# Kernel tuning notes

Hardware: AMD Instinct MI355X
Metric: run time of the kernel (lower is better)

The kernel has to match this reference:

```python
import jax, jax.numpy as jnp
import numpy as np

EPS = 1e-16


def _grads4(x):
    """Four directional shift-differences with zero 'same' padding.

    Matches the fixed 3x3 depthwise conv kernels (cross-correlation):
      Gy: x[i-1,j]   - x[i+1,j]
      Gx: x[i,j-1]   - x[i,j+1]
      GD: x[i-1,j-1] - x[i+1,j+1]
      Gd: x[i-1,j+1] - x[i+1,j-1]
    x: [B, C, H, W]
    """
    B, C, H, W = x.shape
    xp = jnp.pad(x, ((0, 0), (0, 0), (1, 1), (1, 1)))  # zero pad like padding='same'
    gy = xp[:, :, 0:H,     1:W + 1] - xp[:, :, 2:H + 2, 1:W + 1]
    gx = xp[:, :, 1:H + 1, 0:W]     - xp[:, :, 1:H + 1, 2:W + 2]
    gD = xp[:, :, 0:H,     0:W]     - xp[:, :, 2:H + 2, 2:W + 2]
    gd = xp[:, :, 0:H,     2:W + 2] - xp[:, :, 2:H + 2, 0:W]
    return jnp.concatenate([gy, gx, gD, gd], axis=1)  # [B, 4C, H, W]


def setup_inputs() -> dict:
    key = jax.random.key(0)
    k1, k2 = jax.random.split(key)
    shape = (16, 6, 512, 512)
    outputs = jax.random.normal(k1, shape, dtype=jnp.float32)
    labels = jax.random.normal(k2, shape, dtype=jnp.float32)
    return {"outputs": outputs, "labels": labels}


def reference(outputs, labels):
    g_out = _grads4(outputs)
    g_lab = _grads4(labels)
    l1 = jnp.mean(jnp.abs(g_out - g_lab))
    return jnp.sqrt(l1 + EPS)
```

## Files before the change

### kernel.cpp

```cpp
#include <hip/hip_runtime.h>
#include <math.h>


#define NTHREADS 256
#define STRIP 8
#define WV 512
#define HT 512
#define PLANES 96
#define STRIPS_PER_PLANE (HT / STRIP)
#define TOTAL_WAVES (PLANES * STRIPS_PER_PLANE)
#define NBLOCKS (TOTAL_WAVES / (NTHREADS / 64))

struct Row {
    float d[8];
    float eL, eR;
};

__device__ __forceinline__ Row load_row(const float* __restrict__ ob,
                                         const float* __restrict__ lb,
                                         int r, int lane) {
    Row row;
    const size_t off = (size_t)r * WV;
    const float4 o0 = *reinterpret_cast<const float4*>(ob + off);
    const float4 o1 = *reinterpret_cast<const float4*>(ob + off + 4);
    const float4 l0 = *reinterpret_cast<const float4*>(lb + off);
    const float4 l1 = *reinterpret_cast<const float4*>(lb + off + 4);
    row.d[0] = o0.x - l0.x; row.d[1] = o0.y - l0.y;
    row.d[2] = o0.z - l0.z; row.d[3] = o0.w - l0.w;
    row.d[4] = o1.x - l1.x; row.d[5] = o1.y - l1.y;
    row.d[6] = o1.z - l1.z; row.d[7] = o1.w - l1.w;
    const float up = __shfl_up(row.d[7], 1, 64);
    const float dn = __shfl_down(row.d[0], 1, 64);
    row.eL = (lane == 0) ? 0.f : up;
    row.eR = (lane == 63) ? 0.f : dn;
    return row;
}

__device__ __forceinline__ Row zero_row() {
    Row row;
    #pragma unroll
    for (int k = 0; k < 8; ++k) row.d[k] = 0.f;
    row.eL = 0.f; row.eR = 0.f;
    return row;
}

__global__ __launch_bounds__(NTHREADS) void struct_loss_partial(
        const float* __restrict__ out_p, const float* __restrict__ lab_p,
        float* __restrict__ partial) {
    const int gwave = (blockIdx.x * NTHREADS + threadIdx.x) >> 6;
    const int lane  = threadIdx.x & 63;
    const int plane = gwave >> 6;
    const int row0  = (gwave & 63) * STRIP;

    const size_t base = (size_t)plane * (HT * WV) + lane * 8;
    const float* ob = out_p + base;
    const float* lb = lab_p + base;

    float acc = 0.f;

    Row rp = (row0 > 0) ? load_row(ob, lb, row0 - 1, lane) : zero_row();
    Row rc = load_row(ob, lb, row0, lane);

    #pragma unroll
    for (int rr = 0; rr < STRIP; ++rr) {
        const int r = row0 + rr;
        Row rn = (r + 1 < HT) ? load_row(ob, lb, r + 1, lane) : zero_row();

        #pragma unroll
        for (int k = 0; k < 8; ++k) {
            const float cL = (k > 0) ? rc.d[k - 1] : rc.eL;
            const float cR = (k < 7) ? rc.d[k + 1] : rc.eR;
            const float pL = (k > 0) ? rp.d[k - 1] : rp.eL;
            const float pR = (k < 7) ? rp.d[k + 1] : rp.eR;
            const float nL = (k > 0) ? rn.d[k - 1] : rn.eL;
            const float nR = (k < 7) ? rn.d[k + 1] : rn.eR;

            const float gy = rp.d[k] - rn.d[k];
            const float gx = cL - cR;
            const float gD = pL - nR;
            const float gd = pR - nL;
            acc += fabsf(gy) + fabsf(gx) + fabsf(gD) + fabsf(gd);
        }
        rp = rc;
        rc = rn;
    }

    #pragma unroll
    for (int off = 32; off > 0; off >>= 1)
        acc += __shfl_down(acc, off, 64);

    __shared__ float smem[NTHREADS / 64];
    const int wid = threadIdx.x >> 6;
    if (lane == 0) smem[wid] = acc;
    __syncthreads();
    if (threadIdx.x == 0) {
        float s = 0.f;
        #pragma unroll
        for (int w = 0; w < NTHREADS / 64; ++w) s += smem[w];
        partial[blockIdx.x] = s;
    }
}

__global__ __launch_bounds__(256) void struct_loss_final(
        const float* __restrict__ partial, float* __restrict__ out,
        int nparts, double inv_count) {
    double acc = 0.0;
    for (int i = threadIdx.x; i < nparts; i += blockDim.x)
        acc += (double)partial[i];
    #pragma unroll
    for (int off = 32; off > 0; off >>= 1)
        acc += __shfl_down(acc, off, 64);
    __shared__ double smem[4];
    const int lane = threadIdx.x & 63;
    const int wid  = threadIdx.x >> 6;
    if (lane == 0) smem[wid] = acc;
    __syncthreads();
    if (threadIdx.x == 0) {
        double s = smem[0] + smem[1] + smem[2] + smem[3];
        out[0] = (float)sqrt(s * inv_count + 1e-16);
    }
}

extern "C" void kernel_launch(void* const* d_in, const int* in_sizes, int n_in,
                              void* d_out, int out_size, void* d_ws, size_t ws_size,
                              hipStream_t stream) {
    const float* outputs = (const float*)d_in[0];
    const float* labels  = (const float*)d_in[1];
    float* out = (float*)d_out;
    float* partials = (float*)d_ws;

    const double inv_count = 1.0 / (16.0 * 24.0 * 512.0 * 512.0);

    struct_loss_partial<<<NBLOCKS, NTHREADS, 0, stream>>>(outputs, labels, partials);
    struct_loss_final<<<1, 256, 0, stream>>>(partials, out, NBLOCKS, inv_count);
}
```

Measured before the change: 45.46 us.

## Fuse final reduction via last-block atomic, prefetch rows ahead, halve strip height

Merges the separate final-reduction kernel into the main kernel with a threadfence plus atomic counter, so the last finishing block sums the partials; a memset resets the counter each call. Row loads are now issued one row ahead of their conversion to overlap memory latency with compute. Strip height drops from 8 to 4, doubling the wave count, which adds more occupancy but also more redundant halo-row loads. It also adds a memset launch and atomic serialization at the end.

```diff
diff --git a/kernel.cpp b/kernel.cpp
--- a/kernel.cpp
+++ b/kernel.cpp
@@ -3,32 +3,34 @@
 
 
 #define NTHREADS 256
-#define STRIP 8
+#define STRIP 4
 #define WV 512
 #define HT 512
 #define PLANES 96
-#define STRIPS_PER_PLANE (HT / STRIP)
-#define TOTAL_WAVES (PLANES * STRIPS_PER_PLANE)
+#define WAVES_PER_PLANE (HT / STRIP)
+#define TOTAL_WAVES (PLANES * WAVES_PER_PLANE)
 #define NBLOCKS (TOTAL_WAVES / (NTHREADS / 64))
 
-struct Row {
-    float d[8];
-    float eL, eR;
-};
+struct Raw { float4 o0, o1, l0, l1; };
+struct Row { float d[8]; float eL, eR; };
 
-__device__ __forceinline__ Row load_row(const float* __restrict__ ob,
-                                         const float* __restrict__ lb,
-                                         int r, int lane) {
+__device__ __forceinline__ Raw load_raw(const float* __restrict__ ob,
+                                        const float* __restrict__ lb, int r) {
+    Raw w;
+    const size_t off = (size_t)r * WV;
+    w.o0 = *reinterpret_cast<const float4*>(ob + off);
+    w.o1 = *reinterpret_cast<const float4*>(ob + off + 4);
+    w.l0 = *reinterpret_cast<const float4*>(lb + off);
+    w.l1 = *reinterpret_cast<const float4*>(lb + off + 4);
+    return w;
+}
+
+__device__ __forceinline__ Row convert(const Raw& w, int lane) {
     Row row;
-    const size_t off = (size_t)r * WV;
-    const float4 o0 = *reinterpret_cast<const float4*>(ob + off);
-    const float4 o1 = *reinterpret_cast<const float4*>(ob + off + 4);
-    const float4 l0 = *reinterpret_cast<const float4*>(lb + off);
-    const float4 l1 = *reinterpret_cast<const float4*>(lb + off + 4);
-    row.d[0] = o0.x - l0.x; row.d[1] = o0.y - l0.y;
-    row.d[2] = o0.z - l0.z; row.d[3] = o0.w - l0.w;
-    row.d[4] = o1.x - l1.x; row.d[5] = o1.y - l1.y;
-    row.d[6] = o1.z - l1.z; row.d[7] = o1.w - l1.w;
+    row.d[0] = w.o0.x - w.l0.x; row.d[1] = w.o0.y - w.l0.y;
+    row.d[2] = w.o0.z - w.l0.z; row.d[3] = w.o0.w - w.l0.w;
+    row.d[4] = w.o1.x - w.l1.x; row.d[5] = w.o1.y - w.l1.y;
+    row.d[6] = w.o1.z - w.l1.z; row.d[7] = w.o1.w - w.l1.w;
     const float up = __shfl_up(row.d[7], 1, 64);
     const float dn = __shfl_down(row.d[0], 1, 64);
     row.eL = (lane == 0) ? 0.f : up;
@@ -44,13 +46,14 @@
     return row;
 }
 
-__global__ __launch_bounds__(NTHREADS) void struct_loss_partial(
+__global__ __launch_bounds__(NTHREADS) void struct_loss(
         const float* __restrict__ out_p, const float* __restrict__ lab_p,
-        float* __restrict__ partial) {
+        float* __restrict__ partials, unsigned* __restrict__ counter,
+        float* __restrict__ out, double inv_count) {
     const int gwave = (blockIdx.x * NTHREADS + threadIdx.x) >> 6;
     const int lane  = threadIdx.x & 63;
-    const int plane = gwave >> 6;
-    const int row0  = (gwave & 63) * STRIP;
+    const int plane = gwave >> 7;
+    const int row0  = (gwave & (WAVES_PER_PLANE - 1)) * STRIP;
 
     const size_t base = (size_t)plane * (HT * WV) + lane * 8;
     const float* ob = out_p + base;
@@ -58,13 +61,25 @@
 
     float acc = 0.f;
 
-    Row rp = (row0 > 0) ? load_row(ob, lb, row0 - 1, lane) : zero_row();
-    Row rc = load_row(ob, lb, row0, lane);
+    Raw raw_p, raw_c, raw_n;
+    const bool has_p = (row0 > 0);
+    if (has_p) raw_p = load_raw(ob, lb, row0 - 1);
+    raw_c = load_raw(ob, lb, row0);
+    raw_n = load_raw(ob, lb, row0 + 1);
+
+    Row rp = has_p ? convert(raw_p, lane) : zero_row();
+    Row rc = convert(raw_c, lane);
 
     #pragma unroll
     for (int rr = 0; rr < STRIP; ++rr) {
         const int r = row0 + rr;
-        Row rn = (r + 1 < HT) ? load_row(ob, lb, r + 1, lane) : zero_row();
+
+        Raw raw_n2;
+        const bool has_n2 = (r + 2 < HT);
+        if (has_n2) raw_n2 = load_raw(ob, lb, r + 2);
+
+        Row rn;
+        if (r + 1 < HT) rn = convert(raw_n, lane); else rn = zero_row();
 
         #pragma unroll
         for (int k = 0; k < 8; ++k) {
@@ -83,6 +98,7 @@
         }
         rp = rc;
         rc = rn;
+        raw_n = raw_n2;
     }
 
     #pragma unroll
@@ -93,31 +109,36 @@
     const int wid = threadIdx.x >> 6;
     if (lane == 0) smem[wid] = acc;
     __syncthreads();
+
+    __shared__ bool amLast;
     if (threadIdx.x == 0) {
         float s = 0.f;
         #pragma unroll
         for (int w = 0; w < NTHREADS / 64; ++w) s += smem[w];
-        partial[blockIdx.x] = s;
+        partials[blockIdx.x] = s;
+        __threadfence();
+        const unsigned old = atomicAdd(counter, 1u);
+        amLast = (old == (unsigned)(NBLOCKS - 1));
     }
-}
+    __syncthreads();
 
-__global__ __launch_bounds__(256) void struct_loss_final(
-        const float* __restrict__ partial, float* __restrict__ out,
-        int nparts, double inv_count) {
-    double acc = 0.0;
-    for (int i = threadIdx.x; i < nparts; i += blockDim.x)
-        acc += (double)partial[i];
-    #pragma unroll
-    for (int off = 32; off > 0; off >>= 1)
-        acc += __shfl_down(acc, off, 64);
-    __shared__ double smem[4];
-    const int lane = threadIdx.x & 63;
-    const int wid  = threadIdx.x >> 6;
-    if (lane == 0) smem[wid] = acc;
-    __syncthreads();
-    if (threadIdx.x == 0) {
-        double s = smem[0] + smem[1] + smem[2] + smem[3];
-        out[0] = (float)sqrt(s * inv_count + 1e-16);
+    if (amLast) {
+        __threadfence();
+        double s = 0.0;
+        for (int i = threadIdx.x; i < NBLOCKS; i += NTHREADS)
+            s += (double)partials[i];
+        #pragma unroll
+        for (int off = 32; off > 0; off >>= 1)
+            s += __shfl_down(s, off, 64);
+        __shared__ double dsm[NTHREADS / 64];
+        if (lane == 0) dsm[wid] = s;
+        __syncthreads();
+        if (threadIdx.x == 0) {
+            double t = 0.0;
+            #pragma unroll
+            for (int w = 0; w < NTHREADS / 64; ++w) t += dsm[w];
+            out[0] = (float)sqrt(t * inv_count + 1e-16);
+        }
     }
 }
 
@@ -127,10 +148,13 @@
     const float* outputs = (const float*)d_in[0];
     const float* labels  = (const float*)d_in[1];
     float* out = (float*)d_out;
-    float* partials = (float*)d_ws;
+
+    unsigned* counter = (unsigned*)d_ws;
+    float* partials   = (float*)d_ws + 16;
 
     const double inv_count = 1.0 / (16.0 * 24.0 * 512.0 * 512.0);
 
-    struct_loss_partial<<<NBLOCKS, NTHREADS, 0, stream>>>(outputs, labels, partials);
-    struct_loss_final<<<1, 256, 0, stream>>>(partials, out, NBLOCKS, inv_count);
+    hipMemsetAsync(counter, 0, sizeof(unsigned), stream);
+    struct_loss<<<NBLOCKS, NTHREADS, 0, stream>>>(outputs, labels, partials,
+                                                  counter, out, inv_count);
 }
```

After: 143.6 us. 3.16x slower.

## Stage block row tiles with halo in LDS to cut redundant halo reads

Applied to the files above, without the earlier changes.

Each block now loads a 16-row strip plus two halo rows of the output-minus-label difference into shared memory with coalesced float4 loads, then each wave computes four rows from LDS. This lowers redundant global reads of halo rows compared with per-wave 8-row strips and issues all global loads up front. It adds a 36KB LDS footprint per block, a barrier, and an occupancy limit.

```diff
diff --git a/kernel.cpp b/kernel.cpp
--- a/kernel.cpp
+++ b/kernel.cpp
@@ -3,68 +3,78 @@
 
 
 #define NTHREADS 256
-#define STRIP 8
+#define TROWS 16
+#define SROWS (TROWS + 2)
 #define WV 512
 #define HT 512
 #define PLANES 96
-#define STRIPS_PER_PLANE (HT / STRIP)
-#define TOTAL_WAVES (PLANES * STRIPS_PER_PLANE)
-#define NBLOCKS (TOTAL_WAVES / (NTHREADS / 64))
+#define STRIPS (HT / TROWS)
+#define NBLOCKS (PLANES * STRIPS)
+#define F4_PER_TILE (SROWS * WV / 4)
+#define LD_PER_THREAD (F4_PER_TILE / NTHREADS)
 
-struct Row {
-    float d[8];
-    float eL, eR;
-};
+struct Row { float d[8]; float eL, eR; };
 
-__device__ __forceinline__ Row load_row(const float* __restrict__ ob,
-                                         const float* __restrict__ lb,
-                                         int r, int lane) {
+__device__ __forceinline__ Row lds_row(const float* __restrict__ sd,
+                                       int sr, int lane) {
     Row row;
-    const size_t off = (size_t)r * WV;
-    const float4 o0 = *reinterpret_cast<const float4*>(ob + off);
-    const float4 o1 = *reinterpret_cast<const float4*>(ob + off + 4);
-    const float4 l0 = *reinterpret_cast<const float4*>(lb + off);
-    const float4 l1 = *reinterpret_cast<const float4*>(lb + off + 4);
-    row.d[0] = o0.x - l0.x; row.d[1] = o0.y - l0.y;
-    row.d[2] = o0.z - l0.z; row.d[3] = o0.w - l0.w;
-    row.d[4] = o1.x - l1.x; row.d[5] = o1.y - l1.y;
-    row.d[6] = o1.z - l1.z; row.d[7] = o1.w - l1.w;
+    const float4 a = *reinterpret_cast<const float4*>(sd + sr * WV + lane * 8);
+    const float4 b = *reinterpret_cast<const float4*>(sd + sr * WV + lane * 8 + 4);
+    row.d[0] = a.x; row.d[1] = a.y; row.d[2] = a.z; row.d[3] = a.w;
+    row.d[4] = b.x; row.d[5] = b.y; row.d[6] = b.z; row.d[7] = b.w;
     const float up = __shfl_up(row.d[7], 1, 64);
     const float dn = __shfl_down(row.d[0], 1, 64);
-    row.eL = (lane == 0) ? 0.f : up;
+    row.eL = (lane == 0)  ? 0.f : up;
     row.eR = (lane == 63) ? 0.f : dn;
     return row;
 }
 
-__device__ __forceinline__ Row zero_row() {
-    Row row;
+__global__ __launch_bounds__(NTHREADS, 4) void struct_loss_partial(
+        const float* __restrict__ out_p, const float* __restrict__ lab_p,
+        float* __restrict__ partials) {
+    __shared__ float sd[SROWS * WV];
+
+    const int plane = blockIdx.x >> 5;
+    const int strip = blockIdx.x & (STRIPS - 1);
+    const int row0  = strip * TROWS;
+    const size_t pbase = (size_t)plane * (HT * WV);
+
+    float4 ov[LD_PER_THREAD], lv[LD_PER_THREAD];
     #pragma unroll
-    for (int k = 0; k < 8; ++k) row.d[k] = 0.f;
-    row.eL = 0.f; row.eR = 0.f;
-    return row;
-}
+    for (int k = 0; k < LD_PER_THREAD; ++k) {
+        const int p  = threadIdx.x + NTHREADS * k;
+        const int r  = p >> 7;
+        const int c4 = p & 127;
+        const int gr = row0 + r - 1;
+        const int grc = min(max(gr, 0), HT - 1);
+        const size_t goff = pbase + (size_t)grc * WV + c4 * 4;
+        ov[k] = *reinterpret_cast<const float4*>(out_p + goff);
+        lv[k] = *reinterpret_cast<const float4*>(lab_p + goff);
+    }
+    #pragma unroll
+    for (int k = 0; k < LD_PER_THREAD; ++k) {
+        const int p = threadIdx.x + NTHREADS * k;
+        const int r = p >> 7;
+        const int gr = row0 + r - 1;
+        const float m = (gr >= 0 && gr < HT) ? 1.f : 0.f;
+        float4 d;
+        d.x = m * (ov[k].x - lv[k].x);
+        d.y = m * (ov[k].y - lv[k].y);
+        d.z = m * (ov[k].z - lv[k].z);
+        d.w = m * (ov[k].w - lv[k].w);
+        *reinterpret_cast<float4*>(sd + (size_t)p * 4) = d;
+    }
+    __syncthreads();
 
-__global__ __launch_bounds__(NTHREADS) void struct_loss_partial(
-        const float* __restrict__ out_p, const float* __restrict__ lab_p,
-        float* __restrict__ partial) {
-    const int gwave = (blockIdx.x * NTHREADS + threadIdx.x) >> 6;
-    const int lane  = threadIdx.x & 63;
-    const int plane = gwave >> 6;
-    const int row0  = (gwave & 63) * STRIP;
-
-    const size_t base = (size_t)plane * (HT * WV) + lane * 8;
-    const float* ob = out_p + base;
-    const float* lb = lab_p + base;
-
+    const int wv   = threadIdx.x >> 6;
+    const int lane = threadIdx.x & 63;
     float acc = 0.f;
 
-    Row rp = (row0 > 0) ? load_row(ob, lb, row0 - 1, lane) : zero_row();
-    Row rc = load_row(ob, lb, row0, lane);
-
+    Row rp = lds_row(sd, wv * 4,     lane);
+    Row rc = lds_row(sd, wv * 4 + 1, lane);
     #pragma unroll
-    for (int rr = 0; rr < STRIP; ++rr) {
-        const int r = row0 + rr;
-        Row rn = (r + 1 < HT) ? load_row(ob, lb, r + 1, lane) : zero_row();
+    for (int rr = 0; rr < 4; ++rr) {
+        Row rn = lds_row(sd, wv * 4 + 2 + rr, lane);
 
         #pragma unroll
         for (int k = 0; k < 8; ++k) {
@@ -90,14 +100,13 @@
         acc += __shfl_down(acc, off, 64);
 
     __shared__ float smem[NTHREADS / 64];
-    const int wid = threadIdx.x >> 6;
-    if (lane == 0) smem[wid] = acc;
+    if (lane == 0) smem[wv] = acc;
     __syncthreads();
     if (threadIdx.x == 0) {
         float s = 0.f;
         #pragma unroll
         for (int w = 0; w < NTHREADS / 64; ++w) s += smem[w];
-        partial[blockIdx.x] = s;
+        partials[blockIdx.x] = s;
     }
 }
 
```

Measured after the change: 42.17 us. 1.08x faster.
